# Optimization experiments

Measured on AMD Instinct MI355X. Metric: run time of the kernel, lower is better.

The kernel has to match this reference:

```python
import jax, jax.numpy as jnp
import numpy as np

B, L, M, K = 2, 2048, 16, 32
NUM_RBF = 16
MAX_REL = 32  # max_relative_feature in PositionalEncodings


def _linear(x, W, b):
    return x @ W.T + b


def _layernorm(x, g, b, eps=1e-5):
    mu = x.mean(-1, keepdims=True)
    var = ((x - mu) ** 2).mean(-1, keepdims=True)
    return (x - mu) * jax.lax.rsqrt(var + eps) * g + b


def _rbf(D):
    mu = jnp.linspace(2.0, 22.0, NUM_RBF)
    sigma = (22.0 - 2.0) / NUM_RBF
    return jnp.exp(-(((D[..., None] - mu) / sigma) ** 2))


def _gather_edges(feat, E_idx):
    # feat [B,L,L,C], E_idx [B,L,K] -> [B,L,K,C]
    return jnp.take_along_axis(feat, E_idx[..., None], axis=2)


def _dist(Xc, mask, eps=1e-6):
    mask2 = mask[:, :, None] * mask[:, None, :]
    dX = Xc[:, :, None, :] - Xc[:, None, :, :]
    D = mask2 * jnp.sqrt(jnp.sum(dX * dX, -1) + eps)
    D_max = jnp.max(D, -1, keepdims=True)
    D_adj = D + (1.0 - mask2) * D_max
    negD, E_idx = jax.lax.top_k(-D_adj, K)
    return -negD, E_idx


def _get_rbf(A, Bc, E_idx):
    D = jnp.sqrt(jnp.sum((A[:, :, None, :] - Bc[:, None, :, :]) ** 2, -1) + 1e-6)
    return _rbf(_gather_edges(D[..., None], E_idx)[..., 0])


def _angle_features(A, Bc, C, Y):
    v1, v2 = A - Bc, C - Bc
    e1 = v1 / (jnp.linalg.norm(v1, axis=-1, keepdims=True) + 1e-8)
    u2 = v2 - e1 * jnp.sum(e1 * v2, -1, keepdims=True)
    e2 = u2 / (jnp.linalg.norm(u2, axis=-1, keepdims=True) + 1e-8)
    e3 = jnp.cross(e1, e2)
    R = jnp.stack([e1, e2, e3], axis=-1)  # [B,L,3,3]
    lv = jnp.einsum('blqp,blyq->blyp', R, Y - Bc[:, :, None, :])
    rxy = jnp.sqrt(lv[..., 0] ** 2 + lv[..., 1] ** 2 + 1e-8)
    rxyz = jnp.linalg.norm(lv, axis=-1) + 1e-8
    return jnp.stack([lv[..., 0] / rxy, lv[..., 1] / rxy, rxy / rxyz, lv[..., 2] / rxyz], axis=-1)


def setup_inputs() -> dict:
    key = jax.random.key(0)
    ks = jax.random.split(key, 16)
    X = 10.0 * jax.random.normal(ks[0], (B, L, 4, 3), jnp.float32)
    Y = 10.0 * jax.random.normal(ks[1], (B, L, M, 3), jnp.float32)
    Y_t = jax.random.randint(ks[2], (B, L, M), 0, 120)
    Y_m = jnp.ones((B, L, M), jnp.float32)
    mask = jnp.ones((B, L), jnp.float32)
    R_idx = jnp.tile(jnp.arange(L, dtype=jnp.int32)[None], (B, 1))
    chain_labels = jax.random.randint(ks[3], (B, L), 0, 4)
    periodic_table = jnp.stack([
        jnp.arange(120, dtype=jnp.int32),
        jax.random.randint(ks[4], (120,), 0, 19),  # group
        jax.random.randint(ks[5], (120,), 0, 8),   # period
    ])
    s = 0.05
    def w(k, shape):
        return s * jax.random.normal(k, shape, jnp.float32)
    return dict(
        X=X, Y=Y, Y_m=Y_m, mask=mask,
        W_pos=w(ks[6], (16, 66)), b_pos=jnp.zeros(16),
        W_edge=w(ks[7], (128, 416)), b_edge=jnp.zeros(128),
        g_edge=jnp.ones(128), be_edge=jnp.zeros(128),
        W_down=w(ks[8], (128, 148)), b_down=jnp.zeros(128),
        g_node=jnp.ones(128), bn_node=jnp.zeros(128),
        W_type=w(ks[9], (64, 147)), b_type=jnp.zeros(64),
        W_yn=w(ks[10], (128, 147)), b_yn=jnp.zeros(128),
        g_yn=jnp.ones(128), bn_yn=jnp.zeros(128),
        W_ye=w(ks[11], (128, 16)), b_ye=jnp.zeros(128),
        g_ye=jnp.ones(128), bn_ye=jnp.zeros(128),
        Y_t=Y_t, R_idx=R_idx, chain_labels=chain_labels, periodic_table=periodic_table)


def reference(X, Y, Y_m, mask, W_pos, b_pos, W_edge, b_edge, g_edge, be_edge,
              W_down, b_down, g_node, bn_node, W_type, b_type,
              W_yn, b_yn, g_yn, bn_yn, W_ye, b_ye, g_ye, bn_ye,
              Y_t, R_idx, chain_labels, periodic_table):
    N = X[:, :, 0, :]; Ca = X[:, :, 1, :]; C = X[:, :, 2, :]; O = X[:, :, 3, :]
    b_ = Ca - N; c_ = C - Ca; a_ = jnp.cross(b_, c_)
    Cb = -0.58273431 * a_ + 0.56802827 * b_ - 0.54067466 * c_ + Ca
    D_neighbors, E_idx = _dist(Ca, mask)
    pairs = [(N, N), (C, C), (O, O), (Cb, Cb), (Ca, N), (Ca, C), (Ca, O), (Ca, Cb),
             (N, C), (N, O), (N, Cb), (Cb, C), (Cb, O), (O, C), (N, Ca), (C, Ca),
             (O, Ca), (Cb, Ca), (C, N), (O, N), (Cb, N), (C, Cb), (O, Cb), (C, O)]
    RBF_all = jnp.concatenate([_rbf(D_neighbors)] + [_get_rbf(a, bb, E_idx) for a, bb in pairs], axis=-1)
    offset = _gather_edges((R_idx[:, :, None] - R_idx[:, None, :])[..., None], E_idx)[..., 0]
    d_chains = (chain_labels[:, :, None] == chain_labels[:, None, :]).astype(jnp.int32)
    E_chains = _gather_edges(d_chains[..., None], E_idx)[..., 0]
    d = jnp.clip(offset + MAX_REL, 0, 2 * MAX_REL) * E_chains + (1 - E_chains) * (2 * MAX_REL + 1)
    E_pos = _linear(jax.nn.one_hot(d, 2 * MAX_REL + 2, dtype=jnp.float32), W_pos, b_pos)
    E = _layernorm(_linear(jnp.concatenate([E_pos, RBF_all], -1), W_edge, b_edge), g_edge, be_edge)
    Y_t = Y_t.astype(jnp.int32)
    Y_t_1hot_full = jnp.concatenate([
        jax.nn.one_hot(Y_t, 120, dtype=jnp.float32),
        jax.nn.one_hot(periodic_table[1][Y_t], 19, dtype=jnp.float32),
        jax.nn.one_hot(periodic_table[2][Y_t], 8, dtype=jnp.float32)], -1)
    Y_t_proj = _linear(Y_t_1hot_full, W_type, b_type)
    def rbf_to_Y(A):
        return _rbf(jnp.sqrt(jnp.sum((A[:, :, None, :] - Y) ** 2, -1) + 1e-6))
    f_angles = _angle_features(N, Ca, C, Y)
    D_all = jnp.concatenate([rbf_to_Y(N), rbf_to_Y(Ca), rbf_to_Y(C), rbf_to_Y(O), rbf_to_Y(Cb), Y_t_proj, f_angles], -1)
    V = _layernorm(_linear(D_all, W_down, b_down), g_node, bn_node)
    Y_edges = _rbf(jnp.sqrt(jnp.sum((Y[:, :, :, None, :] - Y[:, :, None, :, :]) ** 2, -1) + 1e-6))
    Y_edges = _layernorm(_linear(Y_edges, W_ye, b_ye), g_ye, bn_ye)
    Y_nodes = _layernorm(_linear(Y_t_1hot_full, W_yn, b_yn), g_yn, bn_yn)
    return (V, E, E_idx, Y_nodes, Y_edges, Y_m)
```

## Files before the change

### kernel.cpp

```cpp
#include <hip/hip_runtime.h>
#include <math.h>

#define BB 2
#define LL 2048
#define MM 16
#define KNN 32

#define OFF_V    0
#define OFF_E    8388608
#define OFF_EIDX 25165824
#define OFF_YN   25296896
#define OFF_YE   33685504
#define OFF_YM   167903232

__device__ const int PAIR_A[24] = {0,2,3,4,1,1,1,1,0,0,0,4,4,3,0,2,3,4,2,3,4,2,3,2};
__device__ const int PAIR_B[24] = {0,2,3,4,0,2,3,4,2,3,4,2,3,2,1,1,1,1,0,0,0,4,4,3};

template<int R>
__device__ inline void ln_stats(const float (*o)[129], float (*stat)[2], int t)
{
    constexpr int G = 256 / R;
    constexpr int C = 128 / G;
    const int k = t / G, sub = t % G;
    const float* orow = o[k];
    float s = 0.0f;
    #pragma unroll
    for (int c = 0; c < C; ++c) s += orow[c*G + sub];
    #pragma unroll
    for (int off = G/2; off > 0; off >>= 1) s += __shfl_xor(s, off, 64);
    const float mu = s * 0.0078125f;
    float v = 0.0f;
    #pragma unroll
    for (int c = 0; c < C; ++c) { float d = orow[c*G + sub] - mu; v = fmaf(d, d, v); }
    #pragma unroll
    for (int off = G/2; off > 0; off >>= 1) v += __shfl_xor(v, off, 64);
    if (sub == 0) {
        stat[k][0] = mu;
        stat[k][1] = rsqrtf(v * 0.0078125f + 1e-5f);
    }
}

__global__ __launch_bounds__(256) void prep_kernel(
    const float* __restrict__ Wedge, const float* __restrict__ Wdown,
    const float* __restrict__ X, const float* __restrict__ mask,
    float* __restrict__ WtE, float* __restrict__ WtD, float* __restrict__ Cb,
    float4* __restrict__ CaM)
{
    int idx = blockIdx.x * 256 + threadIdx.x;
    if (idx < 53248) {
        int f = idx >> 7, c = idx & 127;
        WtE[idx] = Wedge[c * 416 + f];
    } else if (idx < 53248 + 18944) {
        int k = idx - 53248;
        int f = k >> 7, c = k & 127;
        WtD[k] = Wdown[c * 148 + f];
    } else if (idx < 53248 + 18944 + BB * LL) {
        int r = idx - 53248 - 18944;
        float Nx = X[r*12+0], Ny = X[r*12+1], Nz = X[r*12+2];
        float Ax = X[r*12+3], Ay = X[r*12+4], Az = X[r*12+5];
        float Cx = X[r*12+6], Cy = X[r*12+7], Cz = X[r*12+8];
        float bx = Ax - Nx, by = Ay - Ny, bz = Az - Nz;
        float cx = Cx - Ax, cy = Cy - Ay, cz = Cz - Az;
        float ax = by * cz - bz * cy;
        float ay = bz * cx - bx * cz;
        float az = bx * cy - by * cx;
        Cb[r*3+0] = -0.58273431f*ax + 0.56802827f*bx - 0.54067466f*cx + Ax;
        Cb[r*3+1] = -0.58273431f*ay + 0.56802827f*by - 0.54067466f*cy + Ay;
        Cb[r*3+2] = -0.58273431f*az + 0.56802827f*bz - 0.54067466f*cz + Az;
    } else if (idx < 53248 + 18944 + 2 * BB * LL) {
        int r = idx - 53248 - 18944 - BB * LL;
        float4 v;
        v.x = X[r*12+3]; v.y = X[r*12+4]; v.z = X[r*12+5]; v.w = mask[r];
        CaM[r] = v;
    }
}

__global__ __launch_bounds__(256) void knn_kernel(
    const float4* __restrict__ CaM,
    int* __restrict__ eidx, float* __restrict__ dn, float* __restrict__ out)
{
    const int row = blockIdx.x;
    const int t = threadIdx.x;
    const int b = row >> 11;
    const int lane = t & 63;
    const int wid = t >> 6;

    __shared__ float wmaxs[4];
    __shared__ unsigned long long wmin[2][4];

    const float4 me = CaM[row];
    float dd[8];
    float m2v[8];
    float lmax = -1e30f;
    #pragma unroll
    for (int s = 0; s < 8; ++s) {
        float4 o4 = CaM[b*LL + s*256 + t];
        float dx = me.x - o4.x, dy = me.y - o4.y, dz = me.z - o4.z;
        float m2 = me.w * o4.w;
        float D = m2 * sqrtf(dx*dx + dy*dy + dz*dz + 1e-6f);
        dd[s] = D;
        m2v[s] = m2;
        lmax = fmaxf(lmax, D);
    }
    #pragma unroll
    for (int off = 32; off > 0; off >>= 1)
        lmax = fmaxf(lmax, __shfl_xor(lmax, off, 64));
    if (lane == 0) wmaxs[wid] = lmax;
    __syncthreads();
    const float Dmax = fmaxf(fmaxf(wmaxs[0], wmaxs[1]), fmaxf(wmaxs[2], wmaxs[3]));

    unsigned long long key[8];
    unsigned long long lmin = ~0ull;
    #pragma unroll
    for (int s = 0; s < 8; ++s) {
        float adj = fmaf(1.0f - m2v[s], Dmax, dd[s]);
        key[s] = ((unsigned long long)__float_as_uint(adj) << 32)
               | (unsigned long long)(unsigned)(s*256 + t);
        lmin = key[s] < lmin ? key[s] : lmin;
    }
    unsigned long long wm = lmin;
    #pragma unroll
    for (int off = 32; off > 0; off >>= 1) {
        unsigned long long o = __shfl_xor(wm, off, 64);
        wm = o < wm ? o : wm;
    }
    if (lane == 0) wmin[0][wid] = wm;
    __syncthreads();

    int p = 0;
    for (int sel = 0; sel < KNN; ++sel) {
        unsigned long long g = wmin[p][0];
        g = wmin[p][1] < g ? wmin[p][1] : g;
        g = wmin[p][2] < g ? wmin[p][2] : g;
        g = wmin[p][3] < g ? wmin[p][3] : g;
        if (t == 0) {
            int j = (int)(g & 0x7ff);
            eidx[row*KNN + sel] = j;
            dn[row*KNN + sel] = __uint_as_float((unsigned)(g >> 32));
            out[OFF_EIDX + row*KNN + sel] = (float)j;
        }
        if (sel == KNN - 1) break;
        const int jwin = (int)(g & 0x7ff);
        const int wwid = (jwin & 255) >> 6;
        if (wid == wwid) {
            #pragma unroll
            for (int s = 0; s < 8; ++s) key[s] = (key[s] == g) ? ~0ull : key[s];
            unsigned long long m = key[0];
            #pragma unroll
            for (int s = 1; s < 8; ++s) m = key[s] < m ? key[s] : m;
            #pragma unroll
            for (int off = 32; off > 0; off >>= 1) {
                unsigned long long o = __shfl_xor(m, off, 64);
                m = o < m ? o : m;
            }
            wm = m;
        }
        if (lane == 0) wmin[p^1][wid] = wm;
        __syncthreads();
        p ^= 1;
    }
}

__global__ __launch_bounds__(256) void edge_kernel(
    const float* __restrict__ X, const float* __restrict__ Cb,
    const int* __restrict__ Ridx, const int* __restrict__ chains,
    const float* __restrict__ Wpos, const float* __restrict__ bpos,
    const float* __restrict__ Wt, const float* __restrict__ bedge,
    const float* __restrict__ ge, const float* __restrict__ be,
    const int* __restrict__ eidx, const float* __restrict__ dn,
    float* __restrict__ out)
{
    const int row = blockIdx.x;
    const int t = threadIdx.x;
    const int b = row >> 11;
    __shared__ __attribute__((aligned(16))) float smem[KNN*420];
    float (*feat)[420] = (float(*)[420])smem;
    float (*o)[129] = (float(*)[129])smem;
    __shared__ float jat[KNN][15];
    __shared__ float dd[KNN][25];
    __shared__ float iat[15];
    __shared__ int   jd[KNN];
    __shared__ float stat[KNN][2];

    if (t < 12) iat[t] = X[row*12 + t];
    else if (t < 15) iat[t] = Cb[row*3 + (t-12)];
    if (t < KNN) {
        int j = eidx[row*KNN + t];
        int gj = b*LL + j;
        #pragma unroll
        for (int q = 0; q < 12; ++q) jat[t][q] = X[gj*12 + q];
        jat[t][12] = Cb[gj*3+0];
        jat[t][13] = Cb[gj*3+1];
        jat[t][14] = Cb[gj*3+2];
        int off = Ridx[row] - Ridx[gj];
        int dcl = off + 32;
        dcl = dcl < 0 ? 0 : (dcl > 64 ? 64 : dcl);
        jd[t] = (chains[row] == chains[gj]) ? dcl : 65;
        dd[t][0] = dn[row*KNN + t];
    }
    __syncthreads();
    for (int idx = t; idx < 24*KNN; idx += 256) {
        int k = idx & (KNN-1);
        int gp = idx >> 5;
        int a = PAIR_A[gp], b2 = PAIR_B[gp];
        float dx = iat[a*3+0] - jat[k][b2*3+0];
        float dy = iat[a*3+1] - jat[k][b2*3+1];
        float dz = iat[a*3+2] - jat[k][b2*3+2];
        dd[k][gp+1] = sqrtf(dx*dx + dy*dy + dz*dz + 1e-6f);
    }
    __syncthreads();
    for (int idx = t; idx < KNN*400; idx += 256) {
        int k = idx / 400;
        int f = idx - k*400;
        float d = dd[k][f >> 4];
        int r = f & 15;
        float z = (d - (2.0f + 1.3333333333f*(float)r)) * 0.8f;
        feat[k][16 + f] = expf(-z*z);
    }
    for (int idx = t; idx < KNN*16; idx += 256) {
        int k = idx >> 4, p = idx & 15;
        feat[k][p] = Wpos[p*66 + jd[k]] + bpos[p];
    }
    __syncthreads();
    const int c2 = (t & 63) * 2;
    const int g4 = t >> 6;
    float acc[8][2];
    #pragma unroll
    for (int r = 0; r < 8; ++r) { acc[r][0] = bedge[c2]; acc[r][1] = bedge[c2+1]; }
    for (int f = 0; f < 416; f += 4) {
        const float2 w0 = *(const float2*)&Wt[(f+0)*128 + c2];
        const float2 w1 = *(const float2*)&Wt[(f+1)*128 + c2];
        const float2 w2 = *(const float2*)&Wt[(f+2)*128 + c2];
        const float2 w3 = *(const float2*)&Wt[(f+3)*128 + c2];
        #pragma unroll
        for (int r = 0; r < 8; ++r) {
            const float4 fv = *(const float4*)&feat[g4*8 + r][f];
            acc[r][0] = fmaf(fv.x, w0.x, acc[r][0]);
            acc[r][0] = fmaf(fv.y, w1.x, acc[r][0]);
            acc[r][0] = fmaf(fv.z, w2.x, acc[r][0]);
            acc[r][0] = fmaf(fv.w, w3.x, acc[r][0]);
            acc[r][1] = fmaf(fv.x, w0.y, acc[r][1]);
            acc[r][1] = fmaf(fv.y, w1.y, acc[r][1]);
            acc[r][1] = fmaf(fv.z, w2.y, acc[r][1]);
            acc[r][1] = fmaf(fv.w, w3.y, acc[r][1]);
        }
    }
    __syncthreads();
    #pragma unroll
    for (int r = 0; r < 8; ++r) {
        o[g4*8 + r][c2]   = acc[r][0];
        o[g4*8 + r][c2+1] = acc[r][1];
    }
    __syncthreads();
    ln_stats<KNN>(o, stat, t);
    __syncthreads();
    const size_t base = (size_t)OFF_E + (size_t)row * KNN * 128;
    for (int idx = t; idx < KNN*128; idx += 256) {
        int k = idx >> 7, c = idx & 127;
        out[base + idx] = (o[k][c] - stat[k][0]) * stat[k][1] * ge[c] + be[c];
    }
}

__global__ __launch_bounds__(256) void node_kernel(
    const float* __restrict__ X, const float* __restrict__ CbA,
    const float* __restrict__ Yp, const int* __restrict__ Yt,
    const int* __restrict__ ptab,
    const float* __restrict__ Wtype, const float* __restrict__ btype,
    const float* __restrict__ WtD, const float* __restrict__ bdown,
    const float* __restrict__ gnode, const float* __restrict__ bnnode,
    const float* __restrict__ Wyn, const float* __restrict__ byn,
    const float* __restrict__ gyn, const float* __restrict__ bnyn,
    float* __restrict__ out)
{
    const int row = blockIdx.x;
    const int t = threadIdx.x;
    __shared__ float atoms[5][3];
    __shared__ float evec[3][3];
    __shared__ float Ys[MM][3];
    __shared__ float dst[5][MM];
    __shared__ __attribute__((aligned(16))) float feat[MM][152];
    __shared__ float o[MM][129];
    __shared__ float stat[MM][2];
    __shared__ int tinfo[MM][3];

    if (t < 12) atoms[t/3][t%3] = X[row*12 + t];
    else if (t < 15) atoms[4][t-12] = CbA[row*3 + (t-12)];
    if (t >= 16 && t < 64) { int q = t - 16; Ys[q/3][q%3] = Yp[row*48 + q]; }
    if (t >= 64 && t < 80) {
        int m = t - 64;
        int ty = Yt[row*16 + m];
        tinfo[m][0] = ty;
        tinfo[m][1] = ptab[120 + ty];
        tinfo[m][2] = ptab[240 + ty];
    }
    __syncthreads();
    if (t == 0) {
        float v1x = atoms[0][0]-atoms[1][0], v1y = atoms[0][1]-atoms[1][1], v1z = atoms[0][2]-atoms[1][2];
        float v2x = atoms[2][0]-atoms[1][0], v2y = atoms[2][1]-atoms[1][1], v2z = atoms[2][2]-atoms[1][2];
        float n1 = sqrtf(v1x*v1x + v1y*v1y + v1z*v1z) + 1e-8f;
        float e1x = v1x/n1, e1y = v1y/n1, e1z = v1z/n1;
        float dp = e1x*v2x + e1y*v2y + e1z*v2z;
        float u2x = v2x - e1x*dp, u2y = v2y - e1y*dp, u2z = v2z - e1z*dp;
        float n2 = sqrtf(u2x*u2x + u2y*u2y + u2z*u2z) + 1e-8f;
        float e2x = u2x/n2, e2y = u2y/n2, e2z = u2z/n2;
        evec[0][0] = e1x; evec[0][1] = e1y; evec[0][2] = e1z;
        evec[1][0] = e2x; evec[1][1] = e2y; evec[1][2] = e2z;
        evec[2][0] = e1y*e2z - e1z*e2y;
        evec[2][1] = e1z*e2x - e1x*e2z;
        evec[2][2] = e1x*e2y - e1y*e2x;
    }
    if (t >= 128 && t < 208) {
        int q = t - 128;
        int a = q >> 4, m = q & 15;
        float dx = atoms[a][0]-Ys[m][0];
        float dy = atoms[a][1]-Ys[m][1];
        float dz = atoms[a][2]-Ys[m][2];
        dst[a][m] = sqrtf(dx*dx + dy*dy + dz*dz + 1e-6f);
    }
    __syncthreads();
    for (int idx = t; idx < 5*16*16; idx += 256) {
        int a = idx >> 8, m = (idx >> 4) & 15, r = idx & 15;
        float z = (dst[a][m] - (2.0f + 1.3333333333f*(float)r)) * 0.8f;
        feat[m][a*16 + r] = expf(-z*z);
    }
    for (int idx = t; idx < 1024; idx += 256) {
        int m = idx >> 6, c = idx & 63;
        const float* wr = Wtype + c*147;
        feat[m][80 + c] = wr[tinfo[m][0]] + wr[120 + tinfo[m][1]] + wr[139 + tinfo[m][2]] + btype[c];
    }
    if (t < 16) {
        int m = t;
        float dx = Ys[m][0]-atoms[1][0], dy = Ys[m][1]-atoms[1][1], dz = Ys[m][2]-atoms[1][2];
        float l0 = evec[0][0]*dx + evec[0][1]*dy + evec[0][2]*dz;
        float l1 = evec[1][0]*dx + evec[1][1]*dy + evec[1][2]*dz;
        float l2 = evec[2][0]*dx + evec[2][1]*dy + evec[2][2]*dz;
        float rxy  = sqrtf(l0*l0 + l1*l1 + 1e-8f);
        float rxyz = sqrtf(l0*l0 + l1*l1 + l2*l2) + 1e-8f;
        feat[m][144] = l0 / rxy;
        feat[m][145] = l1 / rxy;
        feat[m][146] = rxy / rxyz;
        feat[m][147] = l2 / rxyz;
    }
    __syncthreads();
    const int c2 = (t & 63) * 2;
    const int g4 = t >> 6;
    float acc[4][2];
    #pragma unroll
    for (int r = 0; r < 4; ++r) { acc[r][0] = bdown[c2]; acc[r][1] = bdown[c2+1]; }
    for (int f = 0; f < 148; f += 4) {
        const float2 w0 = *(const float2*)&WtD[(f+0)*128 + c2];
        const float2 w1 = *(const float2*)&WtD[(f+1)*128 + c2];
        const float2 w2 = *(const float2*)&WtD[(f+2)*128 + c2];
        const float2 w3 = *(const float2*)&WtD[(f+3)*128 + c2];
        #pragma unroll
        for (int r = 0; r < 4; ++r) {
            const float4 fv = *(const float4*)&feat[g4*4 + r][f];
            acc[r][0] = fmaf(fv.x, w0.x, acc[r][0]);
            acc[r][0] = fmaf(fv.y, w1.x, acc[r][0]);
            acc[r][0] = fmaf(fv.z, w2.x, acc[r][0]);
            acc[r][0] = fmaf(fv.w, w3.x, acc[r][0]);
            acc[r][1] = fmaf(fv.x, w0.y, acc[r][1]);
            acc[r][1] = fmaf(fv.y, w1.y, acc[r][1]);
            acc[r][1] = fmaf(fv.z, w2.y, acc[r][1]);
            acc[r][1] = fmaf(fv.w, w3.y, acc[r][1]);
        }
    }
    #pragma unroll
    for (int r = 0; r < 4; ++r) {
        o[g4*4 + r][c2]   = acc[r][0];
        o[g4*4 + r][c2+1] = acc[r][1];
    }
    __syncthreads();
    ln_stats<MM>(o, stat, t);
    __syncthreads();
    const size_t vbase = (size_t)OFF_V + (size_t)row * 2048;
    for (int idx = t; idx < 2048; idx += 256) {
        int k = idx >> 7, c = idx & 127;
        out[vbase + idx] = (o[k][c] - stat[k][0]) * stat[k][1] * gnode[c] + bnnode[c];
    }
    __syncthreads();
    for (int idx = t; idx < 2048; idx += 256) {
        int m = idx >> 7, c = idx & 127;
        const float* wr = Wyn + c*147;
        o[m][c] = wr[tinfo[m][0]] + wr[120 + tinfo[m][1]] + wr[139 + tinfo[m][2]] + byn[c];
    }
    __syncthreads();
    ln_stats<MM>(o, stat, t);
    __syncthreads();
    const size_t ybase = (size_t)OFF_YN + (size_t)row * 2048;
    for (int idx = t; idx < 2048; idx += 256) {
        int k = idx >> 7, c = idx & 127;
        out[ybase + idx] = (o[k][c] - stat[k][0]) * stat[k][1] * gyn[c] + bnyn[c];
    }
}

__global__ __launch_bounds__(256) void yedge_kernel(
    const float* __restrict__ Yp, const float* __restrict__ Wye,
    const float* __restrict__ bye, const float* __restrict__ gye,
    const float* __restrict__ bnye, float* __restrict__ out)
{
    const int blk = blockIdx.x;
    const int row = blk >> 2;
    const int r0 = (blk & 3) * 64;
    const int t = threadIdx.x;
    __shared__ float Ys[MM][3];
    __shared__ __attribute__((aligned(16))) float Wt[16][128];
    __shared__ __attribute__((aligned(16))) float feat[64][20];
    __shared__ float o[64][129];
    __shared__ float stat[64][2];

    if (t < 48) Ys[t/3][t%3] = Yp[row*48 + t];
    for (int idx = t; idx < 2048; idx += 256) {
        int c = idx & 127, f = idx >> 7;
        Wt[f][c] = Wye[c*16 + f];
    }
    __syncthreads();
    for (int idx = t; idx < 64*16; idx += 256) {
        int r = idx >> 4, rr = idx & 15;
        int gr = r0 + r;
        int m1 = gr >> 4, m2 = gr & 15;
        float dx = Ys[m1][0]-Ys[m2][0];
        float dy = Ys[m1][1]-Ys[m2][1];
        float dz = Ys[m1][2]-Ys[m2][2];
        float d = sqrtf(dx*dx + dy*dy + dz*dz + 1e-6f);
        float z = (d - (2.0f + 1.3333333333f*(float)rr)) * 0.8f;
        feat[r][rr] = expf(-z*z);
    }
    __syncthreads();
    const int c2 = (t & 63) * 2;
    const int g4 = t >> 6;
    float acc[16][2];
    #pragma unroll
    for (int r = 0; r < 16; ++r) { acc[r][0] = bye[c2]; acc[r][1] = bye[c2+1]; }
    #pragma unroll
    for (int f = 0; f < 16; f += 4) {
        const float2 w0 = *(const float2*)&Wt[f+0][c2];
        const float2 w1 = *(const float2*)&Wt[f+1][c2];
        const float2 w2 = *(const float2*)&Wt[f+2][c2];
        const float2 w3 = *(const float2*)&Wt[f+3][c2];
        #pragma unroll
        for (int r = 0; r < 16; ++r) {
            const float4 fv = *(const float4*)&feat[g4*16 + r][f];
            acc[r][0] = fmaf(fv.x, w0.x, acc[r][0]);
            acc[r][0] = fmaf(fv.y, w1.x, acc[r][0]);
            acc[r][0] = fmaf(fv.z, w2.x, acc[r][0]);
            acc[r][0] = fmaf(fv.w, w3.x, acc[r][0]);
            acc[r][1] = fmaf(fv.x, w0.y, acc[r][1]);
            acc[r][1] = fmaf(fv.y, w1.y, acc[r][1]);
            acc[r][1] = fmaf(fv.z, w2.y, acc[r][1]);
            acc[r][1] = fmaf(fv.w, w3.y, acc[r][1]);
        }
    }
    #pragma unroll
    for (int r = 0; r < 16; ++r) {
        o[g4*16 + r][c2]   = acc[r][0];
        o[g4*16 + r][c2+1] = acc[r][1];
    }
    __syncthreads();
    ln_stats<64>(o, stat, t);
    __syncthreads();
    const size_t base = (size_t)OFF_YE + ((size_t)row * 256 + r0) * 128;
    for (int idx = t; idx < 64*128; idx += 256) {
        int k = idx >> 7, c = idx & 127;
        out[base + idx] = (o[k][c] - stat[k][0]) * stat[k][1] * gye[c] + bnye[c];
    }
}

extern "C" void kernel_launch(void* const* d_in, const int* in_sizes, int n_in,
                              void* d_out, int out_size, void* d_ws, size_t ws_size,
                              hipStream_t stream) {
    (void)in_sizes; (void)n_in; (void)out_size; (void)ws_size;
    const float* X      = (const float*)d_in[0];
    const float* Y      = (const float*)d_in[1];
    const float* Y_m    = (const float*)d_in[2];
    const float* mask   = (const float*)d_in[3];
    const float* W_pos  = (const float*)d_in[4];
    const float* b_pos  = (const float*)d_in[5];
    const float* W_edge = (const float*)d_in[6];
    const float* b_edge = (const float*)d_in[7];
    const float* g_edge = (const float*)d_in[8];
    const float* be_edge= (const float*)d_in[9];
    const float* W_down = (const float*)d_in[10];
    const float* b_down = (const float*)d_in[11];
    const float* g_node = (const float*)d_in[12];
    const float* bn_node= (const float*)d_in[13];
    const float* W_type = (const float*)d_in[14];
    const float* b_type = (const float*)d_in[15];
    const float* W_yn   = (const float*)d_in[16];
    const float* b_yn   = (const float*)d_in[17];
    const float* g_yn   = (const float*)d_in[18];
    const float* bn_yn  = (const float*)d_in[19];
    const float* W_ye   = (const float*)d_in[20];
    const float* b_ye   = (const float*)d_in[21];
    const float* g_ye   = (const float*)d_in[22];
    const float* bn_ye  = (const float*)d_in[23];
    const int* Y_t      = (const int*)d_in[24];
    const int* R_idx    = (const int*)d_in[25];
    const int* chains   = (const int*)d_in[26];
    const int* ptab     = (const int*)d_in[27];

    float* out = (float*)d_out;
    float* ws  = (float*)d_ws;
    float* WtE = ws;
    float* WtD = ws + 53248;
    float* Cb  = ws + 72192;
    int*   eidx = (int*)(ws + 84480);
    float* dn  = ws + 215552;

    float* CaM = out + OFF_YE;

    prep_kernel<<<314, 256, 0, stream>>>(W_edge, W_down, X, mask, WtE, WtD, Cb,
                                         (float4*)CaM);
    knn_kernel<<<BB*LL, 256, 0, stream>>>((const float4*)CaM, eidx, dn, out);
    edge_kernel<<<BB*LL, 256, 0, stream>>>(X, Cb, R_idx, chains, W_pos, b_pos,
                                           WtE, b_edge, g_edge, be_edge, eidx, dn, out);
    node_kernel<<<BB*LL, 256, 0, stream>>>(X, Cb, Y, Y_t, ptab, W_type, b_type,
                                           WtD, b_down, g_node, bn_node,
                                           W_yn, b_yn, g_yn, bn_yn, out);
    yedge_kernel<<<BB*LL*4, 256, 0, stream>>>(Y, W_ye, b_ye, g_ye, bn_ye, out);
    hipMemcpyAsync(out + OFF_YM, Y_m, (size_t)BB*LL*MM*sizeof(float),
                   hipMemcpyDeviceToDevice, stream);
}
```

Measured before the change: 1.182 ms.

## Fuse LayerNorm into GEMM epilogue via wave shuffles, prefetch weights

Replaces the shared-memory staging of the linear outputs plus the separate LayerNorm stats pass with an in-register LayerNorm. Each 64-lane wave owns one row's 128 channels (two per lane), so mean and variance come from wave-wide shuffle reductions and results are written straight out as float2. This removes several __syncthreads and LDS round-trips in the edge, node and yedge kernels, and cuts LDS usage, which may raise occupancy. It also software-prefetches the next weight group in the edge and node GEMM loops, at some cost in extra registers.

```diff
diff --git a/kernel.cpp b/kernel.cpp
--- a/kernel.cpp
+++ b/kernel.cpp
@@ -16,28 +16,10 @@
 __device__ const int PAIR_A[24] = {0,2,3,4,1,1,1,1,0,0,0,4,4,3,0,2,3,4,2,3,4,2,3,2};
 __device__ const int PAIR_B[24] = {0,2,3,4,0,2,3,4,2,3,4,2,3,2,1,1,1,1,0,0,0,4,4,3};
 
-template<int R>
-__device__ inline void ln_stats(const float (*o)[129], float (*stat)[2], int t)
-{
-    constexpr int G = 256 / R;
-    constexpr int C = 128 / G;
-    const int k = t / G, sub = t % G;
-    const float* orow = o[k];
-    float s = 0.0f;
-    #pragma unroll
-    for (int c = 0; c < C; ++c) s += orow[c*G + sub];
-    #pragma unroll
-    for (int off = G/2; off > 0; off >>= 1) s += __shfl_xor(s, off, 64);
-    const float mu = s * 0.0078125f;
-    float v = 0.0f;
-    #pragma unroll
-    for (int c = 0; c < C; ++c) { float d = orow[c*G + sub] - mu; v = fmaf(d, d, v); }
-    #pragma unroll
-    for (int off = G/2; off > 0; off >>= 1) v += __shfl_xor(v, off, 64);
-    if (sub == 0) {
-        stat[k][0] = mu;
-        stat[k][1] = rsqrtf(v * 0.0078125f + 1e-5f);
-    }
+__device__ inline float wave_sum(float s) {
+    #pragma unroll
+    for (int off = 32; off > 0; off >>= 1) s += __shfl_xor(s, off, 64);
+    return s;
 }
 
 __global__ __launch_bounds__(256) void prep_kernel(
@@ -173,14 +155,11 @@
     const int row = blockIdx.x;
     const int t = threadIdx.x;
     const int b = row >> 11;
-    __shared__ __attribute__((aligned(16))) float smem[KNN*420];
-    float (*feat)[420] = (float(*)[420])smem;
-    float (*o)[129] = (float(*)[129])smem;
+    __shared__ __attribute__((aligned(16))) float feat[KNN][420];
     __shared__ float jat[KNN][15];
     __shared__ float dd[KNN][25];
     __shared__ float iat[15];
     __shared__ int   jd[KNN];
-    __shared__ float stat[KNN][2];
 
     if (t < 12) iat[t] = X[row*12 + t];
     else if (t < 15) iat[t] = Cb[row*3 + (t-12)];
@@ -227,11 +206,17 @@
     float acc[8][2];
     #pragma unroll
     for (int r = 0; r < 8; ++r) { acc[r][0] = bedge[c2]; acc[r][1] = bedge[c2+1]; }
+    const float* Wp = Wt + c2;
+    float2 w0 = *(const float2*)&Wp[0];
+    float2 w1 = *(const float2*)&Wp[128];
+    float2 w2 = *(const float2*)&Wp[256];
+    float2 w3 = *(const float2*)&Wp[384];
     for (int f = 0; f < 416; f += 4) {
-        const float2 w0 = *(const float2*)&Wt[(f+0)*128 + c2];
-        const float2 w1 = *(const float2*)&Wt[(f+1)*128 + c2];
-        const float2 w2 = *(const float2*)&Wt[(f+2)*128 + c2];
-        const float2 w3 = *(const float2*)&Wt[(f+3)*128 + c2];
+        const float* nWp = Wp + (f + 4 < 416 ? (size_t)(f+4)*128 : 0);
+        float2 n0 = *(const float2*)&nWp[0];
+        float2 n1 = *(const float2*)&nWp[128];
+        float2 n2 = *(const float2*)&nWp[256];
+        float2 n3 = *(const float2*)&nWp[384];
         #pragma unroll
         for (int r = 0; r < 8; ++r) {
             const float4 fv = *(const float4*)&feat[g4*8 + r][f];
@@ -244,20 +229,21 @@
             acc[r][1] = fmaf(fv.z, w2.y, acc[r][1]);
             acc[r][1] = fmaf(fv.w, w3.y, acc[r][1]);
         }
-    }
-    __syncthreads();
+        w0 = n0; w1 = n1; w2 = n2; w3 = n3;
+    }
+    const float g0 = ge[c2], g1 = ge[c2+1];
+    const float e0 = be[c2], e1 = be[c2+1];
+    const size_t base = (size_t)OFF_E + (size_t)row * KNN * 128;
     #pragma unroll
     for (int r = 0; r < 8; ++r) {
-        o[g4*8 + r][c2]   = acc[r][0];
-        o[g4*8 + r][c2+1] = acc[r][1];
-    }
-    __syncthreads();
-    ln_stats<KNN>(o, stat, t);
-    __syncthreads();
-    const size_t base = (size_t)OFF_E + (size_t)row * KNN * 128;
-    for (int idx = t; idx < KNN*128; idx += 256) {
-        int k = idx >> 7, c = idx & 127;
-        out[base + idx] = (o[k][c] - stat[k][0]) * stat[k][1] * ge[c] + be[c];
+        const int k = g4*8 + r;
+        float mu = wave_sum(acc[r][0] + acc[r][1]) * 0.0078125f;
+        float d0 = acc[r][0] - mu, d1 = acc[r][1] - mu;
+        float rstd = rsqrtf(wave_sum(fmaf(d0, d0, d1*d1)) * 0.0078125f + 1e-5f);
+        float2 ov;
+        ov.x = d0 * rstd * g0 + e0;
+        ov.y = d1 * rstd * g1 + e1;
+        *(float2*)&out[base + k*128 + c2] = ov;
     }
 }
 
@@ -279,8 +265,6 @@
     __shared__ float Ys[MM][3];
     __shared__ float dst[5][MM];
     __shared__ __attribute__((aligned(16))) float feat[MM][152];
-    __shared__ float o[MM][129];
-    __shared__ float stat[MM][2];
     __shared__ int tinfo[MM][3];
 
     if (t < 12) atoms[t/3][t%3] = X[row*12 + t];
@@ -347,11 +331,17 @@
     float acc[4][2];
     #pragma unroll
     for (int r = 0; r < 4; ++r) { acc[r][0] = bdown[c2]; acc[r][1] = bdown[c2+1]; }
+    const float* Wp = WtD + c2;
+    float2 w0 = *(const float2*)&Wp[0];
+    float2 w1 = *(const float2*)&Wp[128];
+    float2 w2 = *(const float2*)&Wp[256];
+    float2 w3 = *(const float2*)&Wp[384];
     for (int f = 0; f < 148; f += 4) {
-        const float2 w0 = *(const float2*)&WtD[(f+0)*128 + c2];
-        const float2 w1 = *(const float2*)&WtD[(f+1)*128 + c2];
-        const float2 w2 = *(const float2*)&WtD[(f+2)*128 + c2];
-        const float2 w3 = *(const float2*)&WtD[(f+3)*128 + c2];
+        const float* nWp = Wp + (f + 4 < 148 ? (size_t)(f+4)*128 : 0);
+        float2 n0 = *(const float2*)&nWp[0];
+        float2 n1 = *(const float2*)&nWp[128];
+        float2 n2 = *(const float2*)&nWp[256];
+        float2 n3 = *(const float2*)&nWp[384];
         #pragma unroll
         for (int r = 0; r < 4; ++r) {
             const float4 fv = *(const float4*)&feat[g4*4 + r][f];
@@ -364,33 +354,45 @@
             acc[r][1] = fmaf(fv.z, w2.y, acc[r][1]);
             acc[r][1] = fmaf(fv.w, w3.y, acc[r][1]);
         }
-    }
-    #pragma unroll
-    for (int r = 0; r < 4; ++r) {
-        o[g4*4 + r][c2]   = acc[r][0];
-        o[g4*4 + r][c2+1] = acc[r][1];
-    }
-    __syncthreads();
-    ln_stats<MM>(o, stat, t);
-    __syncthreads();
-    const size_t vbase = (size_t)OFF_V + (size_t)row * 2048;
-    for (int idx = t; idx < 2048; idx += 256) {
-        int k = idx >> 7, c = idx & 127;
-        out[vbase + idx] = (o[k][c] - stat[k][0]) * stat[k][1] * gnode[c] + bnnode[c];
-    }
-    __syncthreads();
-    for (int idx = t; idx < 2048; idx += 256) {
-        int m = idx >> 7, c = idx & 127;
-        const float* wr = Wyn + c*147;
-        o[m][c] = wr[tinfo[m][0]] + wr[120 + tinfo[m][1]] + wr[139 + tinfo[m][2]] + byn[c];
-    }
-    __syncthreads();
-    ln_stats<MM>(o, stat, t);
-    __syncthreads();
-    const size_t ybase = (size_t)OFF_YN + (size_t)row * 2048;
-    for (int idx = t; idx < 2048; idx += 256) {
-        int k = idx >> 7, c = idx & 127;
-        out[ybase + idx] = (o[k][c] - stat[k][0]) * stat[k][1] * gyn[c] + bnyn[c];
+        w0 = n0; w1 = n1; w2 = n2; w3 = n3;
+    }
+    {
+        const float g0 = gnode[c2], g1 = gnode[c2+1];
+        const float e0 = bnnode[c2], e1 = bnnode[c2+1];
+        const size_t vbase = (size_t)OFF_V + (size_t)row * 2048;
+        #pragma unroll
+        for (int r = 0; r < 4; ++r) {
+            const int k = g4*4 + r;
+            float mu = wave_sum(acc[r][0] + acc[r][1]) * 0.0078125f;
+            float d0 = acc[r][0] - mu, d1 = acc[r][1] - mu;
+            float rstd = rsqrtf(wave_sum(fmaf(d0, d0, d1*d1)) * 0.0078125f + 1e-5f);
+            float2 ov;
+            ov.x = d0 * rstd * g0 + e0;
+            ov.y = d1 * rstd * g1 + e1;
+            *(float2*)&out[vbase + k*128 + c2] = ov;
+        }
+    }
+    {
+        const float g0 = gyn[c2], g1 = gyn[c2+1];
+        const float e0 = bnyn[c2], e1 = bnyn[c2+1];
+        const float b0 = byn[c2], b1 = byn[c2+1];
+        const float* wr0 = Wyn + (size_t)c2 * 147;
+        const float* wr1 = wr0 + 147;
+        const size_t ybase = (size_t)OFF_YN + (size_t)row * 2048;
+        #pragma unroll
+        for (int r = 0; r < 4; ++r) {
+            const int m = g4*4 + r;
+            const int i0 = tinfo[m][0], i1 = tinfo[m][1], i2 = tinfo[m][2];
+            float v0 = wr0[i0] + wr0[120 + i1] + wr0[139 + i2] + b0;
+            float v1 = wr1[i0] + wr1[120 + i1] + wr1[139 + i2] + b1;
+            float mu = wave_sum(v0 + v1) * 0.0078125f;
+            float d0 = v0 - mu, d1 = v1 - mu;
+            float rstd = rsqrtf(wave_sum(fmaf(d0, d0, d1*d1)) * 0.0078125f + 1e-5f);
+            float2 ov;
+            ov.x = d0 * rstd * g0 + e0;
+            ov.y = d1 * rstd * g1 + e1;
+            *(float2*)&out[ybase + m*128 + c2] = ov;
+        }
     }
 }
 
@@ -406,8 +408,6 @@
     __shared__ float Ys[MM][3];
     __shared__ __attribute__((aligned(16))) float Wt[16][128];
     __shared__ __attribute__((aligned(16))) float feat[64][20];
-    __shared__ float o[64][129];
-    __shared__ float stat[64][2];
 
     if (t < 48) Ys[t/3][t%3] = Yp[row*48 + t];
     for (int idx = t; idx < 2048; idx += 256) {
@@ -451,18 +451,19 @@
             acc[r][1] = fmaf(fv.w, w3.y, acc[r][1]);
         }
     }
+    const float g0 = gye[c2], g1 = gye[c2+1];
+    const float e0 = bnye[c2], e1 = bnye[c2+1];
+    const size_t base = (size_t)OFF_YE + ((size_t)row * 256 + r0) * 128;
     #pragma unroll
     for (int r = 0; r < 16; ++r) {
-        o[g4*16 + r][c2]   = acc[r][0];
-        o[g4*16 + r][c2+1] = acc[r][1];
-    }
-    __syncthreads();
-    ln_stats<64>(o, stat, t);
-    __syncthreads();
-    const size_t base = (size_t)OFF_YE + ((size_t)row * 256 + r0) * 128;
-    for (int idx = t; idx < 64*128; idx += 256) {
-        int k = idx >> 7, c = idx & 127;
-        out[base + idx] = (o[k][c] - stat[k][0]) * stat[k][1] * gye[c] + bnye[c];
+        const int k = g4*16 + r;
+        float mu = wave_sum(acc[r][0] + acc[r][1]) * 0.0078125f;
+        float d0 = acc[r][0] - mu, d1 = acc[r][1] - mu;
+        float rstd = rsqrtf(wave_sum(fmaf(d0, d0, d1*d1)) * 0.0078125f + 1e-5f);
+        float2 ov;
+        ov.x = d0 * rstd * g0 + e0;
+        ov.y = d1 * rstd * g1 + e1;
+        *(float2*)&out[base + k*128 + c2] = ov;
     }
 }
 
```

Result: slower. 1.237 ms (+4.7%).
